# Performance work log

Hardware: AMD Instinct MI355X
Metric: run time of the kernel (lower is better)

Reference implementation:

```python
import jax, jax.numpy as jnp
import numpy as np

B, T, C, D = 8, 4096, 1024, 64  # batch, block_size, input_dim, output_dim


def setup_inputs() -> dict:
    key = jax.random.key(0)
    kx, kk, kq, kv = jax.random.split(key, 4)
    s = 1.0 / np.sqrt(C)  # nn.Linear default init range scale
    X = jax.random.normal(kx, (B, T, C), dtype=jnp.float32)
    Wk = jax.random.uniform(kk, (D, C), jnp.float32, -s, s) * 0.01  # key weight scaled by 0.01 per __post_init__
    Wq = jax.random.uniform(kq, (D, C), jnp.float32, -s, s)
    Wv = jax.random.uniform(kv, (D, C), jnp.float32, -s, s)
    return {"X": X, "Wk": Wk, "Wq": Wq, "Wv": Wv}


def reference(X, Wk, Wq, Wv):
    # bias-free linear projections (torch Linear: X @ W.T)
    keys = jnp.einsum('btc,dc->btd', X, Wk)
    queries = jnp.einsum('btc,dc->btd', X, Wq)
    values = jnp.einsum('btc,dc->btd', X, Wv)
    # scaled dot-product logits [B, T, T]
    logits = jnp.einsum('btd,bsd->bts', queries, keys) / jnp.sqrt(jnp.float32(D))
    causal = jnp.tril(jnp.ones((T, T), dtype=bool))
    logits = jnp.where(causal[None, :, :], logits, -jnp.inf)
    affinities = jax.nn.softmax(logits, axis=2)  # dropout_frac=0.0 -> identity
    return jnp.einsum('bts,bsd->btd', affinities, values)
```

## Files before the change

### kernel.cpp

```cpp
#include <hip/hip_runtime.h>


typedef short bf16x8 __attribute__((ext_vector_type(8)));
typedef short bf16x4 __attribute__((ext_vector_type(4)));
typedef float f32x4  __attribute__((ext_vector_type(4)));

static __device__ __forceinline__ short f2bf(float x) {
    union { float f; unsigned u; } v; v.f = x;
    return (short)((v.u + 0x7fffu + ((v.u >> 16) & 1u)) >> 16);
}

__global__ __launch_bounds__(64) void pack_w_kernel(
    const float* __restrict__ Wk, const float* __restrict__ Wq,
    const float* __restrict__ Wv, short* __restrict__ Wp)
{
    const int c    = blockIdx.x;
    const int lane = threadIdx.x;
    const int k2   = c & 1;
    const int m    = (c >> 1) % 3;
    const int ksw  = c / 6;
    const int ks   = ksw & 15;
    const int wq   = ksw >> 4;
    const int l15  = lane & 15;
    const int quad = lane >> 4;
    const float* W = (m == 0) ? Wk : (m == 1) ? Wq : Wv;
    const float sc = (m == 1) ? 0.18033688f : 1.0f;
    const float* p = W + (long)(wq * 16 + l15) * 1024 + ks * 64 + k2 * 32 + quad * 8;
    f32x4 a = *(const f32x4*)(p);
    f32x4 b = *(const f32x4*)(p + 4);
    bf16x8 f;
#pragma unroll
    for (int j = 0; j < 4; ++j) { f[j] = f2bf(a[j] * sc); f[j + 4] = f2bf(b[j] * sc); }
    *(bf16x8*)(Wp + (long)c * 512 + lane * 8) = f;
}

__global__ __launch_bounds__(256, 2) void proj_kernel(
    const float* __restrict__ X,
    const short* __restrict__ Wp,
    short* __restrict__ Kb,
    short* __restrict__ Qb,
    short* __restrict__ Vt)
{
    __shared__ __align__(16) short xs[2][64 * 72];
    const int tid  = threadIdx.x;
    const int w    = tid >> 6;
    const int lane = tid & 63;
    const int l15  = lane & 15;
    const int quad = lane >> 4;
    const int t0   = blockIdx.x * 64;

    const int rowA = tid >> 3, colg = tid & 7;
    const int rowB = rowA + 32;
    const float* xpA = X + (long)(t0 + rowA) * 1024 + colg * 8;
    const float* xpB = X + (long)(t0 + rowB) * 1024 + colg * 8;
    const int lwA = rowA * 72 + colg * 8;
    const int lwB = rowB * 72 + colg * 8;

    const short* wp = Wp + (long)(w * 16) * 6 * 512 + lane * 8;

    f32x4 acc[4][3];
#pragma unroll
    for (int rt = 0; rt < 4; ++rt)
#pragma unroll
        for (int m = 0; m < 3; ++m) { acc[rt][m][0]=0.f; acc[rt][m][1]=0.f; acc[rt][m][2]=0.f; acc[rt][m][3]=0.f; }

    f32x4 xr[2][4];
    bf16x8 wfc[3][2], wfn[3][2];

    {
#pragma unroll
        for (int s = 0; s < 2; ++s) {
            const int k0 = s * 64;
            xr[s][0] = *(const f32x4*)(xpA + k0);
            xr[s][1] = *(const f32x4*)(xpA + k0 + 4);
            xr[s][2] = *(const f32x4*)(xpB + k0);
            xr[s][3] = *(const f32x4*)(xpB + k0 + 4);
        }
#pragma unroll
        for (int m = 0; m < 3; ++m)
#pragma unroll
            for (int k2 = 0; k2 < 2; ++k2)
                wfc[m][k2] = *(const bf16x8*)(wp + (m * 2 + k2) * 512);
        bf16x8 c0, c1;
#pragma unroll
        for (int j = 0; j < 4; ++j) { c0[j] = f2bf(xr[0][0][j]); c0[j+4] = f2bf(xr[0][1][j]);
                                      c1[j] = f2bf(xr[0][2][j]); c1[j+4] = f2bf(xr[0][3][j]); }
        *(bf16x8*)(&xs[0][lwA]) = c0;
        *(bf16x8*)(&xs[0][lwB]) = c1;
    }
    __syncthreads();

#pragma unroll 2
    for (int ks = 0; ks < 16; ++ks) {
        const int buf = ks & 1;
        if (ks < 14) {
            const int k0 = (ks + 2) * 64;
            xr[buf][0] = *(const f32x4*)(xpA + k0);
            xr[buf][1] = *(const f32x4*)(xpA + k0 + 4);
            xr[buf][2] = *(const f32x4*)(xpB + k0);
            xr[buf][3] = *(const f32x4*)(xpB + k0 + 4);
        }
        if (ks < 15) {
            const int cb = (ks + 1) * 6;
#pragma unroll
            for (int m = 0; m < 3; ++m)
#pragma unroll
                for (int k2 = 0; k2 < 2; ++k2)
                    wfn[m][k2] = *(const bf16x8*)(wp + (cb + m * 2 + k2) * 512);
        }
#pragma unroll
        for (int k2 = 0; k2 < 2; ++k2)
#pragma unroll
            for (int rt = 0; rt < 4; ++rt) {
                bf16x8 a = *(const bf16x8*)(&xs[buf][(rt * 16 + l15) * 72 + k2 * 32 + quad * 8]);
#pragma unroll
                for (int m = 0; m < 3; ++m)
                    acc[rt][m] = __builtin_amdgcn_mfma_f32_16x16x32_bf16(a, wfc[m][k2], acc[rt][m], 0, 0, 0);
            }
        if (ks < 15) {
            const int nset = (ks + 1) & 1;
            bf16x8 c0, c1;
#pragma unroll
            for (int j = 0; j < 4; ++j) { c0[j] = f2bf(xr[nset][0][j]); c0[j+4] = f2bf(xr[nset][1][j]);
                                          c1[j] = f2bf(xr[nset][2][j]); c1[j+4] = f2bf(xr[nset][3][j]); }
            *(bf16x8*)(&xs[nset][lwA]) = c0;
            *(bf16x8*)(&xs[nset][lwB]) = c1;
        }
        __syncthreads();
#pragma unroll
        for (int m = 0; m < 3; ++m)
#pragma unroll
            for (int k2 = 0; k2 < 2; ++k2) wfc[m][k2] = wfn[m][k2];
    }

    const int d    = w * 16 + l15;
    const int bidx = t0 >> 12;
#pragma unroll
    for (int rt = 0; rt < 4; ++rt) {
        const int tf = t0 + rt * 16 + quad * 4;
#pragma unroll
        for (int r = 0; r < 4; ++r) Kb[(long)(tf + r) * 64 + d] = f2bf(acc[rt][0][r]);
#pragma unroll
        for (int r = 0; r < 4; ++r) Qb[(long)(tf + r) * 64 + d] = f2bf(acc[rt][1][r]);
        bf16x4 pv;
#pragma unroll
        for (int r = 0; r < 4; ++r) pv[r] = f2bf(acc[rt][2][r]);
        *(bf16x4*)(Vt + ((long)bidx * 64 + d) * 4096 + (tf & 4095)) = pv;
    }
}

__global__ __launch_bounds__(256, 2) void flash_kernel(
    const short* __restrict__ Qb,
    const short* __restrict__ Kb,
    const short* __restrict__ Vt,
    float* __restrict__ Out)
{
    __shared__ __align__(16) char smem[33280];
    short* ps = (short*)smem;
    float* os = (float*)smem;
    float* ls = (float*)(smem + 32768);

    const int tid  = threadIdx.x;
    const int w    = tid >> 6;
    const int lane = tid & 63;
    const int l15  = lane & 15;
    const int quad = lane >> 4;
    const int b    = blockIdx.x & 7;
    const int tile = 127 - (blockIdx.x >> 3);
    const int t0   = tile * 32;

    const int nkb = (t0 >> 6) + 1;
    const int len = (nkb + 3) >> 2;
    const int kb0 = w * len;
    const int kb1 = (kb0 + len < nkb) ? (kb0 + len) : nkb;

    const short* Kbase = Kb + (long)b * 4096 * 64;
    const short* Vbase = Vt + (long)b * 64 * 4096;

    bf16x8 aq[2][2];
#pragma unroll
    for (int q2 = 0; q2 < 2; ++q2) {
        const long qoff = ((long)b * 4096 + t0 + q2 * 16 + l15) * 64;
        aq[q2][0] = *(const bf16x8*)(Qb + qoff + quad * 8);
        aq[q2][1] = *(const bf16x8*)(Qb + qoff + 32 + quad * 8);
    }

    bf16x8 bones;
#pragma unroll
    for (int j = 0; j < 8; ++j) bones[j] = (l15 == 0) ? (short)0x3F80 : (short)0;

    f32x4 o[2][4], lacc[2];
#pragma unroll
    for (int q2 = 0; q2 < 2; ++q2) {
        lacc[q2][0]=0.f; lacc[q2][1]=0.f; lacc[q2][2]=0.f; lacc[q2][3]=0.f;
#pragma unroll
        for (int dt = 0; dt < 4; ++dt) { o[q2][dt][0]=0.f; o[q2][dt][1]=0.f; o[q2][dt][2]=0.f; o[q2][dt][3]=0.f; }
    }

    bf16x8 kc[4][2], kn[4][2];
    if (kb0 < kb1) {
        const int s0 = kb0 << 6;
#pragma unroll
        for (int ct = 0; ct < 4; ++ct) {
            const short* kp = Kbase + (long)(s0 + ct * 16 + l15) * 64 + quad * 8;
            kc[ct][0] = *(const bf16x8*)(kp);
            kc[ct][1] = *(const bf16x8*)(kp + 32);
        }
    }

    short* myps0 = ps + ((w << 1) | 0) * 1152;
    short* myps1 = ps + ((w << 1) | 1) * 1152;

    for (int kb = kb0; kb < kb1; ++kb) {
        const int s0 = kb << 6;

        bf16x8 vf[4][2];
#pragma unroll
        for (int dt = 0; dt < 4; ++dt) {
            const short* vp = Vbase + (long)(dt * 16 + l15) * 4096 + s0 + quad * 8;
            vf[dt][0] = *(const bf16x8*)(vp);
            vf[dt][1] = *(const bf16x8*)(vp + 32);
        }
        if (kb + 1 < kb1) {
            const int sn = s0 + 64;
#pragma unroll
            for (int ct = 0; ct < 4; ++ct) {
                const short* kp = Kbase + (long)(sn + ct * 16 + l15) * 64 + quad * 8;
                kn[ct][0] = *(const bf16x8*)(kp);
                kn[ct][1] = *(const bf16x8*)(kp + 32);
            }
        }

        f32x4 st[2][4];
#pragma unroll
        for (int q2 = 0; q2 < 2; ++q2)
#pragma unroll
            for (int ct = 0; ct < 4; ++ct) {
                f32x4 z; z[0]=0.f; z[1]=0.f; z[2]=0.f; z[3]=0.f;
                z = __builtin_amdgcn_mfma_f32_16x16x32_bf16(aq[q2][0], kc[ct][0], z, 0, 0, 0);
                st[q2][ct] = __builtin_amdgcn_mfma_f32_16x16x32_bf16(aq[q2][1], kc[ct][1], z, 0, 0, 0);
            }
        if (kb == nkb - 1) {
#pragma unroll
            for (int q2 = 0; q2 < 2; ++q2)
#pragma unroll
                for (int ct = 0; ct < 4; ++ct) {
                    const int s = s0 + ct * 16 + l15;
#pragma unroll
                    for (int r = 0; r < 4; ++r)
                        if (s > t0 + q2 * 16 + quad * 4 + r) st[q2][ct][r] = -1e30f;
                }
        }
#pragma unroll
        for (int ct = 0; ct < 4; ++ct)
#pragma unroll
            for (int r = 0; r < 4; ++r) {
                myps0[(quad * 4 + r) * 72 + ct * 16 + l15] =
                    f2bf(__builtin_amdgcn_exp2f(st[0][ct][r]));
                myps1[(quad * 4 + r) * 72 + ct * 16 + l15] =
                    f2bf(__builtin_amdgcn_exp2f(st[1][ct][r]));
            }
        bf16x8 ap[2][2];
        ap[0][0] = *(const bf16x8*)(myps0 + l15 * 72 + quad * 8);
        ap[0][1] = *(const bf16x8*)(myps0 + l15 * 72 + 32 + quad * 8);
        ap[1][0] = *(const bf16x8*)(myps1 + l15 * 72 + quad * 8);
        ap[1][1] = *(const bf16x8*)(myps1 + l15 * 72 + 32 + quad * 8);
#pragma unroll
        for (int q2 = 0; q2 < 2; ++q2) {
            lacc[q2] = __builtin_amdgcn_mfma_f32_16x16x32_bf16(ap[q2][0], bones, lacc[q2], 0, 0, 0);
            lacc[q2] = __builtin_amdgcn_mfma_f32_16x16x32_bf16(ap[q2][1], bones, lacc[q2], 0, 0, 0);
        }
#pragma unroll
        for (int q2 = 0; q2 < 2; ++q2)
#pragma unroll
            for (int dt = 0; dt < 4; ++dt) {
                o[q2][dt] = __builtin_amdgcn_mfma_f32_16x16x32_bf16(ap[q2][0], vf[dt][0], o[q2][dt], 0, 0, 0);
                o[q2][dt] = __builtin_amdgcn_mfma_f32_16x16x32_bf16(ap[q2][1], vf[dt][1], o[q2][dt], 0, 0, 0);
            }
#pragma unroll
        for (int ct = 0; ct < 4; ++ct) { kc[ct][0] = kn[ct][0]; kc[ct][1] = kn[ct][1]; }
    }

    __syncthreads();
#pragma unroll
    for (int q2 = 0; q2 < 2; ++q2) {
#pragma unroll
        for (int dt = 0; dt < 4; ++dt)
#pragma unroll
            for (int r = 0; r < 4; ++r)
                os[w * 2048 + (q2 * 16 + quad * 4 + r) * 64 + dt * 16 + l15] = o[q2][dt][r];
        if (l15 == 0) {
#pragma unroll
            for (int r = 0; r < 4; ++r) ls[w * 32 + q2 * 16 + quad * 4 + r] = lacc[q2][r];
        }
    }
    __syncthreads();

    const int row = tid >> 3, c0 = (tid & 7) * 8;
    f32x4 a0, a1; a0[0]=0.f;a0[1]=0.f;a0[2]=0.f;a0[3]=0.f; a1=a0;
    float lsum = 0.f;
#pragma unroll
    for (int w2 = 0; w2 < 4; ++w2) {
        f32x4 v0 = *(const f32x4*)(os + w2 * 2048 + row * 64 + c0);
        f32x4 v1 = *(const f32x4*)(os + w2 * 2048 + row * 64 + c0 + 4);
        a0[0]+=v0[0]; a0[1]+=v0[1]; a0[2]+=v0[2]; a0[3]+=v0[3];
        a1[0]+=v1[0]; a1[1]+=v1[1]; a1[2]+=v1[2]; a1[3]+=v1[3];
        lsum += ls[w2 * 32 + row];
    }
    const float inv = 1.0f / lsum;
    f32x4 r0, r1;
    r0[0]=a0[0]*inv; r0[1]=a0[1]*inv; r0[2]=a0[2]*inv; r0[3]=a0[3]*inv;
    r1[0]=a1[0]*inv; r1[1]=a1[1]*inv; r1[2]=a1[2]*inv; r1[3]=a1[3]*inv;
    float* op = Out + ((long)b * 4096 + t0 + row) * 64 + c0;
    *(f32x4*)(op)     = r0;
    *(f32x4*)(op + 4) = r1;
}

extern "C" void kernel_launch(void* const* d_in, const int* in_sizes, int n_in,
                              void* d_out, int out_size, void* d_ws, size_t ws_size,
                              hipStream_t stream) {
    const float* X  = (const float*)d_in[0];
    const float* Wk = (const float*)d_in[1];
    const float* Wq = (const float*)d_in[2];
    const float* Wv = (const float*)d_in[3];

    short* ws = (short*)d_ws;
    const long NE = (long)8 * 4096 * 64;
    short* Qb = ws;
    short* Kb = ws + NE;
    short* Vt = ws + 2 * NE;
    short* Wpk = ws + 3 * NE;

    pack_w_kernel<<<384, 64, 0, stream>>>(Wk, Wq, Wv, Wpk);
    proj_kernel<<<512, 256, 0, stream>>>(X, Wpk, Kb, Qb, Vt);
    flash_kernel<<<1024, 256, 0, stream>>>(Qb, Kb, Vt, (float*)d_out);
}
```

Baseline: 273.6 us.

## Replace MFMA row-sum with scalar accumulation, software-pipeline V loads, raise occupancy

The flash kernel now computes the softmax denominator by adding bf16-rounded probabilities in registers and reducing them with cross-lane shuffles at the end, instead of running extra MFMAs against a ones vector. K and V fragments are prefetched one block ahead with reuse of a single register set (V is loaded after the PV MFMAs for the next iteration), and s_setprio brackets the MFMA sections. Launch bounds go from 2 to 3 blocks per CU to increase occupancy. The risks are register spilling under the tighter bound and added VALU work for the row sums.

```diff
diff --git a/kernel.cpp b/kernel.cpp
--- a/kernel.cpp
+++ b/kernel.cpp
@@ -8,6 +8,10 @@
 static __device__ __forceinline__ short f2bf(float x) {
     union { float f; unsigned u; } v; v.f = x;
     return (short)((v.u + 0x7fffu + ((v.u >> 16) & 1u)) >> 16);
+}
+static __device__ __forceinline__ float bf2f(short s) {
+    union { unsigned u; float f; } v; v.u = ((unsigned)(unsigned short)s) << 16;
+    return v.f;
 }
 
 __global__ __launch_bounds__(64) void pack_w_kernel(
@@ -149,7 +153,7 @@
     }
 }
 
-__global__ __launch_bounds__(256, 2) void flash_kernel(
+__global__ __launch_bounds__(256, 3) void flash_kernel(
     const short* __restrict__ Qb,
     const short* __restrict__ Kb,
     const short* __restrict__ Vt,
@@ -185,61 +189,57 @@
         aq[q2][1] = *(const bf16x8*)(Qb + qoff + 32 + quad * 8);
     }
 
-    bf16x8 bones;
-#pragma unroll
-    for (int j = 0; j < 8; ++j) bones[j] = (l15 == 0) ? (short)0x3F80 : (short)0;
-
-    f32x4 o[2][4], lacc[2];
+    f32x4 o[2][4], rs[2];
 #pragma unroll
     for (int q2 = 0; q2 < 2; ++q2) {
-        lacc[q2][0]=0.f; lacc[q2][1]=0.f; lacc[q2][2]=0.f; lacc[q2][3]=0.f;
+        rs[q2][0]=0.f; rs[q2][1]=0.f; rs[q2][2]=0.f; rs[q2][3]=0.f;
 #pragma unroll
         for (int dt = 0; dt < 4; ++dt) { o[q2][dt][0]=0.f; o[q2][dt][1]=0.f; o[q2][dt][2]=0.f; o[q2][dt][3]=0.f; }
     }
 
-    bf16x8 kc[4][2], kn[4][2];
+    bf16x8 kf[4][2], vf[4][2];
     if (kb0 < kb1) {
         const int s0 = kb0 << 6;
 #pragma unroll
         for (int ct = 0; ct < 4; ++ct) {
             const short* kp = Kbase + (long)(s0 + ct * 16 + l15) * 64 + quad * 8;
-            kc[ct][0] = *(const bf16x8*)(kp);
-            kc[ct][1] = *(const bf16x8*)(kp + 32);
+            kf[ct][0] = *(const bf16x8*)(kp);
+            kf[ct][1] = *(const bf16x8*)(kp + 32);
+            const short* vp = Vbase + (long)(ct * 16 + l15) * 4096 + s0 + quad * 8;
+            vf[ct][0] = *(const bf16x8*)(vp);
+            vf[ct][1] = *(const bf16x8*)(vp + 32);
         }
     }
 
     short* myps0 = ps + ((w << 1) | 0) * 1152;
     short* myps1 = ps + ((w << 1) | 1) * 1152;
 
+#pragma unroll 1
     for (int kb = kb0; kb < kb1; ++kb) {
         const int s0 = kb << 6;
 
-        bf16x8 vf[4][2];
-#pragma unroll
-        for (int dt = 0; dt < 4; ++dt) {
-            const short* vp = Vbase + (long)(dt * 16 + l15) * 4096 + s0 + quad * 8;
-            vf[dt][0] = *(const bf16x8*)(vp);
-            vf[dt][1] = *(const bf16x8*)(vp + 32);
-        }
+        f32x4 st[2][4];
+        __builtin_amdgcn_s_setprio(1);
+#pragma unroll
+        for (int q2 = 0; q2 < 2; ++q2)
+#pragma unroll
+            for (int ct = 0; ct < 4; ++ct) {
+                f32x4 z; z[0]=0.f; z[1]=0.f; z[2]=0.f; z[3]=0.f;
+                z = __builtin_amdgcn_mfma_f32_16x16x32_bf16(aq[q2][0], kf[ct][0], z, 0, 0, 0);
+                st[q2][ct] = __builtin_amdgcn_mfma_f32_16x16x32_bf16(aq[q2][1], kf[ct][1], z, 0, 0, 0);
+            }
+        __builtin_amdgcn_s_setprio(0);
+
         if (kb + 1 < kb1) {
             const int sn = s0 + 64;
 #pragma unroll
             for (int ct = 0; ct < 4; ++ct) {
                 const short* kp = Kbase + (long)(sn + ct * 16 + l15) * 64 + quad * 8;
-                kn[ct][0] = *(const bf16x8*)(kp);
-                kn[ct][1] = *(const bf16x8*)(kp + 32);
-            }
-        }
-
-        f32x4 st[2][4];
-#pragma unroll
-        for (int q2 = 0; q2 < 2; ++q2)
-#pragma unroll
-            for (int ct = 0; ct < 4; ++ct) {
-                f32x4 z; z[0]=0.f; z[1]=0.f; z[2]=0.f; z[3]=0.f;
-                z = __builtin_amdgcn_mfma_f32_16x16x32_bf16(aq[q2][0], kc[ct][0], z, 0, 0, 0);
-                st[q2][ct] = __builtin_amdgcn_mfma_f32_16x16x32_bf16(aq[q2][1], kc[ct][1], z, 0, 0, 0);
-            }
+                kf[ct][0] = *(const bf16x8*)(kp);
+                kf[ct][1] = *(const bf16x8*)(kp + 32);
+            }
+        }
+
         if (kb == nkb - 1) {
 #pragma unroll
             for (int q2 = 0; q2 < 2; ++q2)
@@ -251,35 +251,64 @@
                         if (s > t0 + q2 * 16 + quad * 4 + r) st[q2][ct][r] = -1e30f;
                 }
         }
+
 #pragma unroll
         for (int ct = 0; ct < 4; ++ct)
 #pragma unroll
             for (int r = 0; r < 4; ++r) {
-                myps0[(quad * 4 + r) * 72 + ct * 16 + l15] =
-                    f2bf(__builtin_amdgcn_exp2f(st[0][ct][r]));
-                myps1[(quad * 4 + r) * 72 + ct * 16 + l15] =
-                    f2bf(__builtin_amdgcn_exp2f(st[1][ct][r]));
-            }
-        bf16x8 ap[2][2];
-        ap[0][0] = *(const bf16x8*)(myps0 + l15 * 72 + quad * 8);
-        ap[0][1] = *(const bf16x8*)(myps0 + l15 * 72 + 32 + quad * 8);
-        ap[1][0] = *(const bf16x8*)(myps1 + l15 * 72 + quad * 8);
-        ap[1][1] = *(const bf16x8*)(myps1 + l15 * 72 + 32 + quad * 8);
-#pragma unroll
-        for (int q2 = 0; q2 < 2; ++q2) {
-            lacc[q2] = __builtin_amdgcn_mfma_f32_16x16x32_bf16(ap[q2][0], bones, lacc[q2], 0, 0, 0);
-            lacc[q2] = __builtin_amdgcn_mfma_f32_16x16x32_bf16(ap[q2][1], bones, lacc[q2], 0, 0, 0);
-        }
-#pragma unroll
-        for (int q2 = 0; q2 < 2; ++q2)
+                const short p0 = f2bf(__builtin_amdgcn_exp2f(st[0][ct][r]));
+                const short p1 = f2bf(__builtin_amdgcn_exp2f(st[1][ct][r]));
+                myps0[(quad * 4 + r) * 72 + ct * 16 + l15] = p0;
+                myps1[(quad * 4 + r) * 72 + ct * 16 + l15] = p1;
+                rs[0][r] += bf2f(p0);
+                rs[1][r] += bf2f(p1);
+            }
+
+        {
+            bf16x8 ap0 = *(const bf16x8*)(myps0 + l15 * 72 + quad * 8);
+            bf16x8 ap1 = *(const bf16x8*)(myps0 + l15 * 72 + 32 + quad * 8);
+            __builtin_amdgcn_s_setprio(1);
 #pragma unroll
             for (int dt = 0; dt < 4; ++dt) {
-                o[q2][dt] = __builtin_amdgcn_mfma_f32_16x16x32_bf16(ap[q2][0], vf[dt][0], o[q2][dt], 0, 0, 0);
-                o[q2][dt] = __builtin_amdgcn_mfma_f32_16x16x32_bf16(ap[q2][1], vf[dt][1], o[q2][dt], 0, 0, 0);
-            }
-#pragma unroll
-        for (int ct = 0; ct < 4; ++ct) { kc[ct][0] = kn[ct][0]; kc[ct][1] = kn[ct][1]; }
-    }
+                o[0][dt] = __builtin_amdgcn_mfma_f32_16x16x32_bf16(ap0, vf[dt][0], o[0][dt], 0, 0, 0);
+                o[0][dt] = __builtin_amdgcn_mfma_f32_16x16x32_bf16(ap1, vf[dt][1], o[0][dt], 0, 0, 0);
+            }
+            __builtin_amdgcn_s_setprio(0);
+        }
+        {
+            bf16x8 ap0 = *(const bf16x8*)(myps1 + l15 * 72 + quad * 8);
+            bf16x8 ap1 = *(const bf16x8*)(myps1 + l15 * 72 + 32 + quad * 8);
+            __builtin_amdgcn_s_setprio(1);
+#pragma unroll
+            for (int dt = 0; dt < 4; ++dt) {
+                o[1][dt] = __builtin_amdgcn_mfma_f32_16x16x32_bf16(ap0, vf[dt][0], o[1][dt], 0, 0, 0);
+                o[1][dt] = __builtin_amdgcn_mfma_f32_16x16x32_bf16(ap1, vf[dt][1], o[1][dt], 0, 0, 0);
+            }
+            __builtin_amdgcn_s_setprio(0);
+        }
+
+        if (kb + 1 < kb1) {
+            const int sn = s0 + 64;
+#pragma unroll
+            for (int ct = 0; ct < 4; ++ct) {
+                const short* vp = Vbase + (long)(ct * 16 + l15) * 4096 + sn + quad * 8;
+                vf[ct][0] = *(const bf16x8*)(vp);
+                vf[ct][1] = *(const bf16x8*)(vp + 32);
+            }
+        }
+    }
+
+#pragma unroll
+    for (int q2 = 0; q2 < 2; ++q2)
+#pragma unroll
+        for (int r = 0; r < 4; ++r) {
+            float s = rs[q2][r];
+            s += __shfl_xor(s, 1);
+            s += __shfl_xor(s, 2);
+            s += __shfl_xor(s, 4);
+            s += __shfl_xor(s, 8);
+            rs[q2][r] = s;
+        }
 
     __syncthreads();
 #pragma unroll
@@ -291,7 +320,7 @@
                 os[w * 2048 + (q2 * 16 + quad * 4 + r) * 64 + dt * 16 + l15] = o[q2][dt][r];
         if (l15 == 0) {
 #pragma unroll
-            for (int r = 0; r < 4; ++r) ls[w * 32 + q2 * 16 + quad * 4 + r] = lacc[q2][r];
+            for (int r = 0; r < 4; ++r) ls[w * 32 + q2 * 16 + quad * 4 + r] = rs[q2][r];
         }
     }
     __syncthreads();
```

Measured after the change: 294.8 us. +7.7%, slower.
